# Optimization experiments

Hardware: AMD Instinct MI355X
Metric: run time of the kernel (lower is better)

## Reference

```python
import jax, jax.numpy as jnp
import numpy as np

GWIDTH2 = 0.3  # Gaussian bandwidth squared
PNORM = 2


def setup_inputs() -> dict:
    key = jax.random.key(0)
    k1, k2 = jax.random.split(key)
    b, c, h, w = 16, 3, 256, 256
    npro = 32
    x = jax.random.uniform(k1, (b, c, h, w), dtype=jnp.float32)  # pixel values in [0,1]
    P = jax.random.uniform(k2, (npro, c), dtype=jnp.float32)     # p x c prototype pixels
    return {"x": x, "P": P}


def reference(x, P):
    # x: (b, c, h, w); P: (p, c)
    b, c, h, w = x.shape
    # broadcast difference -> (b, p, c, h, w); pnorm=2 distance over channels
    diff = x[:, None, :, :, :] - P[None, :, :, None, None]
    normsp = jnp.sum(diff ** PNORM, axis=2) ** (1.0 / PNORM)  # (b, p, h, w)
    expo = jnp.exp(-normsp / (2.0 * GWIDTH2))
    Y = jnp.sum(expo, axis=(2, 3))  # (b, p)
    return Y / (h * w)
```

## Files before the change

kernel.cpp:

```cpp
#include <hip/hip_runtime.h>


#define NPRO    32
#define HW      65536
#define THREADS 256
#define BPB     32

__global__ __launch_bounds__(THREADS) void soft_count_kernel(
    const float* __restrict__ x, const float* __restrict__ P,
    float* __restrict__ out)
{
    __shared__ float sP[NPRO * 3];
    __shared__ float sred[4][NPRO];

    const float A = 2.4044917f;

    const int tid = threadIdx.x;
    if (tid < NPRO * 3) sP[tid] = P[tid] * A;
    __syncthreads();

    const int b   = blockIdx.x / BPB;
    const int blk = blockIdx.x % BPB;

    const float* base = x + (size_t)b * 3 * HW;

    float rr[8], gg[8], bb[8];
#pragma unroll
    for (int k = 0; k < 2; ++k) {
        const int idx = blk * (THREADS * 8) + k * (THREADS * 4) + tid * 4;
        const float4 r4 = *(const float4*)(base + idx);
        const float4 g4 = *(const float4*)(base + HW + idx);
        const float4 b4 = *(const float4*)(base + 2 * HW + idx);
        rr[k*4+0] = r4.x * A; rr[k*4+1] = r4.y * A; rr[k*4+2] = r4.z * A; rr[k*4+3] = r4.w * A;
        gg[k*4+0] = g4.x * A; gg[k*4+1] = g4.y * A; gg[k*4+2] = g4.z * A; gg[k*4+3] = g4.w * A;
        bb[k*4+0] = b4.x * A; bb[k*4+1] = b4.y * A; bb[k*4+2] = b4.z * A; bb[k*4+3] = b4.w * A;
    }

    float acc[NPRO];
#pragma unroll
    for (int p = 0; p < NPRO; ++p) {
        const float p0 = sP[p * 3 + 0];
        const float p1 = sP[p * 3 + 1];
        const float p2 = sP[p * 3 + 2];
        float s = 0.0f;
#pragma unroll
        for (int j = 0; j < 8; ++j) {
            const float d0 = rr[j] - p0;
            const float d1 = gg[j] - p1;
            const float d2 = bb[j] - p2;
            const float n2 = fmaf(d2, d2, fmaf(d1, d1, d0 * d0));
            s += __builtin_amdgcn_exp2f(-__builtin_amdgcn_sqrtf(n2));
        }
        acc[p] = s;
    }

    const int lane = tid & 63;
    const int wv   = tid >> 6;
#pragma unroll
    for (int p = 0; p < NPRO; ++p) {
        float v = acc[p];
#pragma unroll
        for (int off = 32; off >= 1; off >>= 1)
            v += __shfl_down(v, off, 64);
        if (lane == 0) sred[wv][p] = v;
    }
    __syncthreads();

    if (tid < NPRO) {
        const float v = sred[0][tid] + sred[1][tid] + sred[2][tid] + sred[3][tid];
        atomicAdd(&out[b * NPRO + tid], v * (1.0f / (float)HW));
    }
}

extern "C" void kernel_launch(void* const* d_in, const int* in_sizes, int n_in,
                              void* d_out, int out_size, void* d_ws, size_t ws_size,
                              hipStream_t stream) {
    const float* x = (const float*)d_in[0];
    const float* P = (const float*)d_in[1];
    float* out = (float*)d_out;

    const int nb = in_sizes[0] / (3 * HW);

    hipMemsetAsync(out, 0, (size_t)out_size * sizeof(float), stream);
    soft_count_kernel<<<nb * BPB, THREADS, 0, stream>>>(x, P, out);
}
```

Before: 75.24 us.

## Pack distance math into float2 vectors and use transpose-style butterfly reduction

```diff
diff --git a/kernel.cpp b/kernel.cpp
--- a/kernel.cpp
+++ b/kernel.cpp
@@ -5,6 +5,8 @@
 #define HW      65536
 #define THREADS 256
 #define BPB     32
+
+typedef float v2f __attribute__((ext_vector_type(2)));
 
 __global__ __launch_bounds__(THREADS) void soft_count_kernel(
     const float* __restrict__ x, const float* __restrict__ P,
@@ -24,16 +26,19 @@
 
     const float* base = x + (size_t)b * 3 * HW;
 
-    float rr[8], gg[8], bb[8];
+    v2f r2[4], g2[4], b2[4];
 #pragma unroll
     for (int k = 0; k < 2; ++k) {
         const int idx = blk * (THREADS * 8) + k * (THREADS * 4) + tid * 4;
         const float4 r4 = *(const float4*)(base + idx);
         const float4 g4 = *(const float4*)(base + HW + idx);
         const float4 b4 = *(const float4*)(base + 2 * HW + idx);
-        rr[k*4+0] = r4.x * A; rr[k*4+1] = r4.y * A; rr[k*4+2] = r4.z * A; rr[k*4+3] = r4.w * A;
-        gg[k*4+0] = g4.x * A; gg[k*4+1] = g4.y * A; gg[k*4+2] = g4.z * A; gg[k*4+3] = g4.w * A;
-        bb[k*4+0] = b4.x * A; bb[k*4+1] = b4.y * A; bb[k*4+2] = b4.z * A; bb[k*4+3] = b4.w * A;
+        r2[k*2+0] = (v2f){r4.x * A, r4.y * A};
+        r2[k*2+1] = (v2f){r4.z * A, r4.w * A};
+        g2[k*2+0] = (v2f){g4.x * A, g4.y * A};
+        g2[k*2+1] = (v2f){g4.z * A, g4.w * A};
+        b2[k*2+0] = (v2f){b4.x * A, b4.y * A};
+        b2[k*2+1] = (v2f){b4.z * A, b4.w * A};
     }
 
     float acc[NPRO];
@@ -42,27 +47,45 @@
         const float p0 = sP[p * 3 + 0];
         const float p1 = sP[p * 3 + 1];
         const float p2 = sP[p * 3 + 2];
+        const v2f P0 = (v2f){p0, p0};
+        const v2f P1 = (v2f){p1, p1};
+        const v2f P2 = (v2f){p2, p2};
         float s = 0.0f;
 #pragma unroll
-        for (int j = 0; j < 8; ++j) {
-            const float d0 = rr[j] - p0;
-            const float d1 = gg[j] - p1;
-            const float d2 = bb[j] - p2;
-            const float n2 = fmaf(d2, d2, fmaf(d1, d1, d0 * d0));
-            s += __builtin_amdgcn_exp2f(-__builtin_amdgcn_sqrtf(n2));
+        for (int j = 0; j < 4; ++j) {
+            const v2f d0 = r2[j] - P0;
+            const v2f d1 = g2[j] - P1;
+            const v2f d2 = b2[j] - P2;
+            v2f n2 = d0 * d0;
+            n2 = __builtin_elementwise_fma(d1, d1, n2);
+            n2 = __builtin_elementwise_fma(d2, d2, n2);
+            s += __builtin_amdgcn_exp2f(-__builtin_amdgcn_sqrtf(n2.x));
+            s += __builtin_amdgcn_exp2f(-__builtin_amdgcn_sqrtf(n2.y));
         }
         acc[p] = s;
     }
 
     const int lane = tid & 63;
     const int wv   = tid >> 6;
+    {
+        int n = NPRO;
 #pragma unroll
-    for (int p = 0; p < NPRO; ++p) {
-        float v = acc[p];
+        for (int m = 1; m <= 16; m <<= 1) {
+            n >>= 1;
+            const bool hi = (lane & m) != 0;
 #pragma unroll
-        for (int off = 32; off >= 1; off >>= 1)
-            v += __shfl_down(v, off, 64);
-        if (lane == 0) sred[wv][p] = v;
+            for (int i = 0; i < n; ++i) {
+                const float send = hi ? acc[i] : acc[i + n];
+                const float keep = hi ? acc[i + n] : acc[i];
+                acc[i] = keep + __shfl_xor(send, m, 64);
+            }
+        }
+        acc[0] += __shfl_xor(acc[0], 32, 64);
+    }
+    if (lane < NPRO) {
+        const int proto = ((lane & 1) << 4) | ((lane & 2) << 2) | (lane & 4)
+                        | ((lane & 8) >> 2) | ((lane & 16) >> 4);
+        sred[wv][proto] = acc[0];
     }
     __syncthreads();
 
```

New measurement: 97.44 us. 1.3x slower.
